# Kernel optimization log

Measured on AMD Instinct MI355X. Metric: run time of the kernel, lower is better.

## Reference

```python
import jax, jax.numpy as jnp
import numpy as np

B, T, D, H = 2, 2048, 1024, 16
DH = D // H  # 64


def setup_inputs() -> dict:
    key = jax.random.key(0)
    k1, k2, k3 = jax.random.split(key, 3)
    x = jax.random.normal(k1, (B, T, D), dtype=jnp.float32)
    # torch nn.Linear(d, 3d, bias=False): y = x @ W.T; we store W already transposed as [in, out]
    Wqkv = jax.random.normal(k2, (D, 3 * D), dtype=jnp.float32) * (1.0 / np.sqrt(D))
    Wproj = jax.random.normal(k3, (D, D), dtype=jnp.float32) * (1.0 / np.sqrt(D))
    return {"x": x, "Wqkv": Wqkv, "Wproj": Wproj}


def reference(x, Wqkv, Wproj):
    Bx, Tx, C = x.shape
    qkv = x @ Wqkv                                   # [B,T,3C]
    q, k, v = jnp.split(qkv, 3, axis=-1)
    def rs(t):
        return t.reshape(Bx, Tx, H, DH).transpose(0, 2, 1, 3)  # [B,H,T,DH]
    q, k, v = rs(q), rs(k), rs(v)
    scale = 1.0 / jnp.sqrt(jnp.asarray(DH, dtype=x.dtype))
    att = jnp.einsum('bhqd,bhkd->bhqk', q, k) * scale          # [B,H,T,T]
    causal = jnp.tril(jnp.ones((Tx, Tx), dtype=bool))
    att = jnp.where(causal[None, None, :, :], att, jnp.asarray(-jnp.inf, dtype=att.dtype))
    att = jax.nn.softmax(att, axis=-1)
    out = jnp.einsum('bhqk,bhkd->bhqd', att, v)                # [B,H,T,DH]
    out = out.transpose(0, 2, 1, 3).reshape(Bx, Tx, C)         # [B,T,C]
    return out @ Wproj
```

## Files before the change

kernel.cpp:

```cpp
#include <hip/hip_runtime.h>
#include <hip/hip_bf16.h>

#define BB 2
#define TT 2048
#define DD 1024
#define HH 16
#define MM (BB*TT)
#define N3 (3*DD)
#define QKW 2048

typedef __attribute__((ext_vector_type(8))) short short8;
typedef __attribute__((ext_vector_type(4))) float f32x4;
typedef __attribute__((ext_vector_type(16))) float f32x16;

#define ZERO16 (f32x16){0,0,0,0,0,0,0,0,0,0,0,0,0,0,0,0}

#define GLDS16(g, l) __builtin_amdgcn_global_load_lds( \
    (const __attribute__((address_space(1))) void*)(g), \
    (__attribute__((address_space(3))) void*)(l), 16, 0, 0)

__device__ __forceinline__ unsigned short f2bf(float f) {
    union { float f; unsigned u; } v; v.f = f;
    unsigned r = v.u + 0x7FFFu + ((v.u >> 16) & 1u);
    return (unsigned short)(r >> 16);
}

__device__ __forceinline__ unsigned cvt_pk_bf16(float lo, float hi) {
    unsigned r;
    asm("v_cvt_pk_bf16_f32 %0, %1, %2" : "=v"(r) : "v"(lo), "v"(hi));
    return r;
}

__device__ __forceinline__ float fast_exp2(float x) {
    float r;
    asm("v_exp_f32 %0, %1" : "=v"(r) : "v"(x));
    return r;
}
__device__ __forceinline__ float fast_rcp(float x) {
    float r;
    asm("v_rcp_f32 %0, %1" : "=v"(r) : "v"(x));
    return r;
}

__global__ void prep_kernel(const float* __restrict__ x,
                            const float* __restrict__ Wqkv,
                            const float* __restrict__ Wproj,
                            unsigned short* __restrict__ xb,
                            unsigned short* __restrict__ wqkvt,
                            unsigned short* __restrict__ wprojt) {
    __shared__ float tile[32][33];
    const int bid = blockIdx.x;
    const int tx = threadIdx.x, ty = threadIdx.y;
    if (bid < 4096) {
        const float* src;
        unsigned short* dst;
        int rows, cols, c0, r0;
        if (bid < 3072) {
            src = Wqkv; dst = wqkvt; rows = DD; cols = N3;
            c0 = (bid % 96) * 32; r0 = (bid / 96) * 32;
        } else {
            src = Wproj; dst = wprojt; rows = DD; cols = DD;
            int b2 = bid - 3072;
            c0 = (b2 & 31) * 32; r0 = (b2 >> 5) * 32;
        }
#pragma unroll
        for (int i = 0; i < 4; i++) {
            int r = ty + i * 8;
            tile[r][tx] = src[(size_t)(r0 + r) * cols + c0 + tx];
        }
        __syncthreads();
#pragma unroll
        for (int i = 0; i < 4; i++) {
            int r = ty + i * 8;
            dst[(size_t)(c0 + r) * rows + r0 + tx] = f2bf(tile[tx][r]);
        }
    } else {
        const int t = ty * 32 + tx;
        int i = (bid - 4096) * 256 + t;
        const int n8 = MM * DD / 8;
#pragma unroll
        for (int k = 0; k < 2; k++, i += 262144) {
            const float4* s = reinterpret_cast<const float4*>(x) + (size_t)i * 2;
            float4 a = s[0], b = s[1];
            unsigned short r[8] = {f2bf(a.x), f2bf(a.y), f2bf(a.z), f2bf(a.w),
                                   f2bf(b.x), f2bf(b.y), f2bf(b.z), f2bf(b.w)};
            *reinterpret_cast<uint4*>(xb + (size_t)i * 8) = *reinterpret_cast<uint4*>(r);
            (void)n8;
        }
    }
}

__global__ __launch_bounds__(512, 2)
void gemm256_qkv(const unsigned short* __restrict__ A,
                 const unsigned short* __restrict__ Bt,
                 unsigned short* __restrict__ qkv2,
                 unsigned short* __restrict__ Vout,
                 float scale) {
    __shared__ unsigned short Al[2][2][128][64];
    __shared__ unsigned short Bl[2][2][128][64];

    const int id = blockIdx.y * 12 + blockIdx.x;
    const int swzid = (id & 7) * 24 + (id >> 3);
    const int tm = (swzid / 12) * 256, tn = (swzid % 12) * 256;
    const int t = threadIdx.x, w = t >> 6, l = t & 63;
    const int wm = w >> 2, wn = w & 3, bh = wn >> 1;
    const int lo = l & 15, hi = l >> 4;
    const int srow = l >> 3;
    const int sg = (l & 7) ^ srow;

    f32x4 acc[8][4];
#pragma unroll
    for (int i = 0; i < 8; i++)
#pragma unroll
        for (int j = 0; j < 4; j++) acc[i][j] = (f32x4){0.f, 0.f, 0.f, 0.f};

    const unsigned short* Abase = A + (size_t)(tm + w * 16 + srow) * 1024 + sg * 8;
    const unsigned short* Bbase = Bt + (size_t)(tn + w * 16 + srow) * 1024 + sg * 8;

#define STG_A(KT, H) { \
    GLDS16(Abase + (size_t)(H) * 128 * 1024 + ((KT) & 15) * 64, &Al[(KT) & 1][H][w * 16][0]); \
    GLDS16(Abase + (size_t)(H) * 128 * 1024 + 8 * 1024 + ((KT) & 15) * 64, &Al[(KT) & 1][H][w * 16 + 8][0]); }
#define STG_B(KT, H) { \
    GLDS16(Bbase + (size_t)(H) * 128 * 1024 + ((KT) & 15) * 64, &Bl[(KT) & 1][H][w * 16][0]); \
    GLDS16(Bbase + (size_t)(H) * 128 * 1024 + 8 * 1024 + ((KT) & 15) * 64, &Bl[(KT) & 1][H][w * 16 + 8][0]); }

#define LOAD_A(AFR, KP, MH) { \
    const char* ab = (const char*)&Al[KP][wm][0][0]; \
    _Pragma("unroll") \
    for (int fi = 0; fi < 4; fi++) \
    _Pragma("unroll") \
    for (int ks = 0; ks < 2; ks++) \
        AFR[fi][ks] = *reinterpret_cast<const short8*>( \
            ab + ((MH) * 64 + fi * 16 + lo) * 128 + (((ks * 4 + hi) ^ (lo & 7)) << 4)); }
#define LOAD_B(BFR, KP, NH) { \
    const char* bb = (const char*)&Bl[KP][bh][0][0]; \
    _Pragma("unroll") \
    for (int fj = 0; fj < 2; fj++) \
    _Pragma("unroll") \
    for (int ks = 0; ks < 2; ks++) \
        BFR[fj][ks] = *reinterpret_cast<const short8*>( \
            bb + ((wn & 1) * 64 + (NH) * 32 + fj * 16 + lo) * 128 + (((ks * 4 + hi) ^ (lo & 7)) << 4)); }

#define MFMA16(MH, NH, AFR, BFR) { \
    _Pragma("unroll") \
    for (int ks = 0; ks < 2; ks++) \
    _Pragma("unroll") \
    for (int fi = 0; fi < 4; fi++) \
    _Pragma("unroll") \
    for (int fj = 0; fj < 2; fj++) \
        acc[(MH) * 4 + fi][(NH) * 2 + fj] = __builtin_amdgcn_mfma_f32_16x16x32_bf16( \
            AFR[fi][ks], BFR[fj][ks], acc[(MH) * 4 + fi][(NH) * 2 + fj], 0, 0, 0); }

#define BAR __builtin_amdgcn_s_barrier()
#define LGKM0 asm volatile("s_waitcnt lgkmcnt(0)")
#define P1 __builtin_amdgcn_s_setprio(1)
#define P0 __builtin_amdgcn_s_setprio(0)

    STG_A(0, 0); STG_A(0, 1); STG_B(0, 0); STG_B(0, 1);
    STG_B(1, 0); STG_B(1, 1);
    asm volatile("s_waitcnt vmcnt(4)");
    BAR;

    for (int i = 0; i < 8; i++) {
        const int kt = 2 * i;
        short8 AF[4][2], BA[2][2], BBf[2][2];
        LOAD_A(AF, 0, 0); LOAD_B(BA, 0, 0);
        STG_A(kt + 1, 0); STG_A(kt + 1, 1);
        BAR; LGKM0; P1; MFMA16(0, 0, AF, BA); P0; BAR;
        LOAD_B(BBf, 0, 1);
        BAR; LGKM0; P1; MFMA16(0, 1, AF, BBf); P0; BAR;
        LOAD_A(AF, 0, 1);
        STG_B(kt + 2, 0); STG_B(kt + 2, 1);
        BAR; LGKM0; P1; MFMA16(1, 1, AF, BBf); P0; BAR;
        STG_A(kt + 2, 0);
        BAR; LGKM0; P1; MFMA16(1, 0, AF, BA); P0;
        asm volatile("s_waitcnt vmcnt(6)");
        BAR;
        LOAD_A(AF, 1, 0); LOAD_B(BA, 1, 0);
        STG_A(kt + 2, 1);
        BAR; LGKM0; P1; MFMA16(0, 0, AF, BA); P0; BAR;
        LOAD_B(BBf, 1, 1);
        BAR; LGKM0; P1; MFMA16(0, 1, AF, BBf); P0; BAR;
        LOAD_A(AF, 1, 1);
        STG_B(kt + 3, 0); STG_B(kt + 3, 1);
        BAR; LGKM0; P1; MFMA16(1, 1, AF, BBf); P0; BAR;
        BAR; LGKM0; P1; MFMA16(1, 0, AF, BA); P0;
        asm volatile("s_waitcnt vmcnt(4)");
        BAR;
    }

#pragma unroll
    for (int i = 0; i < 8; i++)
#pragma unroll
        for (int j = 0; j < 4; j++) {
            const int col = tn + wn * 64 + j * 16 + lo;
            const int row0 = tm + wm * 128 + i * 16 + hi * 4;
            if (col < 2 * DD) {
                float s = (col < DD) ? scale : 1.0f;
#pragma unroll
                for (int r = 0; r < 4; r++)
                    qkv2[(size_t)(row0 + r) * QKW + col] = f2bf(acc[i][j][r] * s);
            } else {
                unsigned short pk[4];
#pragma unroll
                for (int r = 0; r < 4; r++) pk[r] = f2bf(acc[i][j][r]);
                *reinterpret_cast<uint2*>(&Vout[(size_t)(col - 2 * DD) * MM + row0]) =
                    *reinterpret_cast<uint2*>(pk);
            }
        }
#undef STG_A
#undef STG_B
#undef LOAD_A
#undef LOAD_B
#undef MFMA16
#undef BAR
#undef LGKM0
#undef P1
#undef P0
}

__global__ __launch_bounds__(256)
void gemm_kernel(const unsigned short* __restrict__ A,
                 const unsigned short* __restrict__ Bt,
                 float* __restrict__ Cout, int M, int N, int K) {
    __shared__ unsigned short As[128][64];
    __shared__ unsigned short Bs[128][64];
    const int nbx = gridDim.x;
    const int id = blockIdx.y * nbx + blockIdx.x;
    const int cpx = (nbx * gridDim.y) >> 3;
    const int swz = (id & 7) * cpx + (id >> 3);
    const int tm = (swz / nbx) * 128, tn = (swz % nbx) * 128;
    const int t = threadIdx.x;
    const int w = t >> 6, lane = t & 63, lo = lane & 15, hi = lane >> 4;
    const int wr = w >> 1, wc = w & 1;

    f32x4 acc[4][4];
#pragma unroll
    for (int i = 0; i < 4; i++)
#pragma unroll
        for (int j = 0; j < 4; j++) acc[i][j] = (f32x4){0.f, 0.f, 0.f, 0.f};

    const int srow = w * 32 + (lane >> 3);
    const int scol = (lane & 7) * 8;
    const unsigned short* ga = &A[(size_t)(tm + srow) * K + scol];
    const unsigned short* gb = &Bt[(size_t)(tn + srow) * K + scol];

    for (int k0 = 0; k0 < K; k0 += 64) {
        __syncthreads();
#pragma unroll
        for (int i = 0; i < 4; i++) {
            GLDS16(ga + (size_t)(i * 8) * K + k0, &As[w * 32 + i * 8][0]);
            GLDS16(gb + (size_t)(i * 8) * K + k0, &Bs[w * 32 + i * 8][0]);
        }
        __syncthreads();

        short8 af[4][2], bf[4][2];
#pragma unroll
        for (int i = 0; i < 4; i++)
#pragma unroll
            for (int ks = 0; ks < 2; ks++) {
                af[i][ks] = *reinterpret_cast<const short8*>(&As[wr * 64 + i * 16 + lo][ks * 32 + hi * 8]);
                bf[i][ks] = *reinterpret_cast<const short8*>(&Bs[wc * 64 + i * 16 + lo][ks * 32 + hi * 8]);
            }
#pragma unroll
        for (int ks = 0; ks < 2; ks++)
#pragma unroll
            for (int i = 0; i < 4; i++)
#pragma unroll
                for (int j = 0; j < 4; j++)
                    acc[i][j] = __builtin_amdgcn_mfma_f32_16x16x32_bf16(af[i][ks], bf[j][ks], acc[i][j], 0, 0, 0);
    }
#pragma unroll
    for (int i = 0; i < 4; i++)
#pragma unroll
        for (int j = 0; j < 4; j++) {
            const int col = tn + wc * 64 + j * 16 + lo;
            const int row0 = tm + wr * 64 + i * 16 + hi * 4;
#pragma unroll
            for (int r = 0; r < 4; r++)
                Cout[(size_t)(row0 + r) * N + col] = acc[i][j][r];
        }
}

__global__ __launch_bounds__(256)
void attn_kernel(const unsigned short* __restrict__ qkv2,
                 const unsigned short* __restrict__ vtg,
                 unsigned short* __restrict__ outp) {
    __shared__ unsigned short Ks[2][64][64];
    __shared__ unsigned short Vt[2][64][64];

    const int b = blockIdx.z, h = blockIdx.x, p = blockIdx.y;
    const int qcl = p, qch = 31 - p;
    const int L = p + 1, Hn = 32 - p;
    const int t = threadIdx.x;
    const int w = t >> 6, l = t & 63, ql = l & 31, hi8 = l >> 5;
    const int pr = w >> 1, rg = w & 1;
    const int q0h = qch * 64 + rg * 32;
    const int q0p = (pr ? qcl : qch) * 64 + rg * 32;
    const unsigned short* base2 = qkv2 + (size_t)b * TT * QKW;

    short8 bq[4];
#pragma unroll
    for (int ks = 0; ks < 4; ks++)
        bq[ks] = *reinterpret_cast<const short8*>(
            &base2[(size_t)(q0p + ql) * QKW + h * 64 + ks * 16 + hi8 * 8]);

    f32x16 o0 = ZERO16, o1 = ZERO16, lD = ZERO16;

    short8 ones1;
#pragma unroll
    for (int j = 0; j < 8; j++) ones1[j] = (short)0x3F80;

    const int krow = l >> 3;
    const int kc8 = (l & 7) ^ krow;
    const unsigned short* gk = &base2[(size_t)(w * 8 + krow) * QKW + DD + h * 64 + kc8 * 8];
    const unsigned short* gv = &vtg[(size_t)(h * 64 + w * 8 + krow) * MM + b * TT + kc8 * 8];

#define STAGE(KVB, BUF) { \
    GLDS16(gk + (size_t)(KVB) * QKW, &Ks[BUF][w * 8][0]); \
    GLDS16(gk + (size_t)((KVB) + 32) * QKW, &Ks[BUF][32 + w * 8][0]); \
    GLDS16(gv + (KVB), &Vt[BUF][w * 8][0]); \
    GLDS16(gv + (size_t)32 * MM + (KVB), &Vt[BUF][32 + w * 8][0]); }

#define WRITE_OUT(Q0) { \
    _Pragma("unroll") \
    for (int r = 0; r < 16; r++) { \
        int src = (r & 3) + 8 * (r >> 2) + 4 * hi8; \
        float inv = fast_rcp(lD[r]); \
        size_t off = (size_t)(b * TT + (Q0) + src) * DD + h * 64 + ql; \
        outp[off] = f2bf(o0[r] * inv); \
        outp[off + 32] = f2bf(o1[r] * inv); \
    } }

    STAGE(0, 0);
    __syncthreads();

    const int sw4 = (ql & 7) << 4;
    int it = 0;
    for (int kvt = 0; kvt < Hn; kvt++, it ^= 1) {
        const bool more = (kvt + 1) < Hn;
        if (more) STAGE((kvt + 1) * 64, it ^ 1);

        if (kvt == L && pr == 1) {
            WRITE_OUT(qcl * 64 + rg * 32);
            o0 = ZERO16; o1 = ZERO16; lD = ZERO16;
#pragma unroll
            for (int ks = 0; ks < 4; ks++)
                bq[ks] = *reinterpret_cast<const short8*>(
                    &base2[(size_t)(q0h + ql) * QKW + h * 64 + ks * 16 + hi8 * 8]);
        }

        const char* kbase = (const char*)&Ks[it][0][0];
        const char* vbase = (const char*)&Vt[it][0][0];
        const int kvb = kvt * 64;

        if (kvt < L) {
            short8 ak0[4], ak1[4];
#pragma unroll
            for (int ks = 0; ks < 4; ks++) {
                ak0[ks] = *reinterpret_cast<const short8*>(kbase + ql * 128 + (((ks * 2 + hi8) << 4) ^ sw4));
                ak1[ks] = *reinterpret_cast<const short8*>(kbase + (32 + ql) * 128 + (((ks * 2 + hi8) << 4) ^ sw4));
            }
            f32x16 sa0 = ZERO16, sa1 = ZERO16;
#pragma unroll
            for (int ks = 0; ks < 4; ks++) {
                sa0 = __builtin_amdgcn_mfma_f32_32x32x16_bf16(ak0[ks], bq[ks], sa0, 0, 0, 0);
                sa1 = __builtin_amdgcn_mfma_f32_32x32x16_bf16(ak1[ks], bq[ks], sa1, 0, 0, 0);
            }
            if (pr == 1 && kvt == L - 1) {
                const int qg = q0p + ql;
#pragma unroll
                for (int r = 0; r < 16; r++) {
                    int crow = (r & 3) + 8 * (r >> 2) + 4 * hi8;
                    if (kvb + crow > qg) sa0[r] = -1e30f;
                    if (kvb + 32 + crow > qg) sa1[r] = -1e30f;
                }
            }
#pragma unroll
            for (int r = 0; r < 16; r++) sa0[r] = fast_exp2(sa0[r]);
#pragma unroll
            for (int r = 0; r < 16; r++) sa1[r] = fast_exp2(sa1[r]);

            unsigned a01 = cvt_pk_bf16(sa0[0], sa0[1]),  a23 = cvt_pk_bf16(sa0[2], sa0[3]);
            unsigned a45 = cvt_pk_bf16(sa0[4], sa0[5]),  a67 = cvt_pk_bf16(sa0[6], sa0[7]);
            asm("v_permlane32_swap_b32 %0, %1" : "+v"(a01), "+v"(a45));
            asm("v_permlane32_swap_b32 %0, %1" : "+v"(a23), "+v"(a67));
            unsigned b01 = cvt_pk_bf16(sa0[8], sa0[9]),  b23 = cvt_pk_bf16(sa0[10], sa0[11]);
            unsigned b45 = cvt_pk_bf16(sa0[12], sa0[13]), b67 = cvt_pk_bf16(sa0[14], sa0[15]);
            asm("v_permlane32_swap_b32 %0, %1" : "+v"(b01), "+v"(b45));
            asm("v_permlane32_swap_b32 %0, %1" : "+v"(b23), "+v"(b67));
            unsigned c01 = cvt_pk_bf16(sa1[0], sa1[1]),  c23 = cvt_pk_bf16(sa1[2], sa1[3]);
            unsigned c45 = cvt_pk_bf16(sa1[4], sa1[5]),  c67 = cvt_pk_bf16(sa1[6], sa1[7]);
            asm("v_permlane32_swap_b32 %0, %1" : "+v"(c01), "+v"(c45));
            asm("v_permlane32_swap_b32 %0, %1" : "+v"(c23), "+v"(c67));
            unsigned d01 = cvt_pk_bf16(sa1[8], sa1[9]),  d23 = cvt_pk_bf16(sa1[10], sa1[11]);
            unsigned d45 = cvt_pk_bf16(sa1[12], sa1[13]), d67 = cvt_pk_bf16(sa1[14], sa1[15]);
            asm("v_permlane32_swap_b32 %0, %1" : "+v"(d01), "+v"(d45));
            asm("v_permlane32_swap_b32 %0, %1" : "+v"(d23), "+v"(d67));
            union { unsigned u[4]; short8 s; } f0s0, f1s0, f0s1, f1s1;
            f0s0.u[0] = a01; f0s0.u[1] = a23; f0s0.u[2] = a45; f0s0.u[3] = a67;
            f1s0.u[0] = b01; f1s0.u[1] = b23; f1s0.u[2] = b45; f1s0.u[3] = b67;
            f0s1.u[0] = c01; f0s1.u[1] = c23; f0s1.u[2] = c45; f0s1.u[3] = c67;
            f1s1.u[0] = d01; f1s1.u[1] = d23; f1s1.u[2] = d45; f1s1.u[3] = d67;

            lD = __builtin_amdgcn_mfma_f32_32x32x16_bf16(f0s0.s, ones1, lD, 0, 0, 0);
            lD = __builtin_amdgcn_mfma_f32_32x32x16_bf16(f1s0.s, ones1, lD, 0, 0, 0);
            lD = __builtin_amdgcn_mfma_f32_32x32x16_bf16(f0s1.s, ones1, lD, 0, 0, 0);
            lD = __builtin_amdgcn_mfma_f32_32x32x16_bf16(f1s1.s, ones1, lD, 0, 0, 0);

            short8 bv00 = *reinterpret_cast<const short8*>(vbase + ql * 128 + (((0 + hi8) << 4) ^ sw4));
            short8 bv01 = *reinterpret_cast<const short8*>(vbase + ql * 128 + (((2 + hi8) << 4) ^ sw4));
            short8 bv02 = *reinterpret_cast<const short8*>(vbase + ql * 128 + (((4 + hi8) << 4) ^ sw4));
            short8 bv03 = *reinterpret_cast<const short8*>(vbase + ql * 128 + (((6 + hi8) << 4) ^ sw4));
            short8 bv10 = *reinterpret_cast<const short8*>(vbase + (32 + ql) * 128 + (((0 + hi8) << 4) ^ sw4));
            short8 bv11 = *reinterpret_cast<const short8*>(vbase + (32 + ql) * 128 + (((2 + hi8) << 4) ^ sw4));
            short8 bv12 = *reinterpret_cast<const short8*>(vbase + (32 + ql) * 128 + (((4 + hi8) << 4) ^ sw4));
            short8 bv13 = *reinterpret_cast<const short8*>(vbase + (32 + ql) * 128 + (((6 + hi8) << 4) ^ sw4));
            o0 = __builtin_amdgcn_mfma_f32_32x32x16_bf16(f0s0.s, bv00, o0, 0, 0, 0);
            o1 = __builtin_amdgcn_mfma_f32_32x32x16_bf16(f0s0.s, bv10, o1, 0, 0, 0);
            o0 = __builtin_amdgcn_mfma_f32_32x32x16_bf16(f1s0.s, bv01, o0, 0, 0, 0);
            o1 = __builtin_amdgcn_mfma_f32_32x32x16_bf16(f1s0.s, bv11, o1, 0, 0, 0);
            o0 = __builtin_amdgcn_mfma_f32_32x32x16_bf16(f0s1.s, bv02, o0, 0, 0, 0);
            o1 = __builtin_amdgcn_mfma_f32_32x32x16_bf16(f0s1.s, bv12, o1, 0, 0, 0);
            o0 = __builtin_amdgcn_mfma_f32_32x32x16_bf16(f1s1.s, bv03, o0, 0, 0, 0);
            o1 = __builtin_amdgcn_mfma_f32_32x32x16_bf16(f1s1.s, bv13, o1, 0, 0, 0);
        } else {
            const int sub = pr;
            short8 ak[4];
#pragma unroll
            for (int ks = 0; ks < 4; ks++)
                ak[ks] = *reinterpret_cast<const short8*>(
                    kbase + (sub * 32 + ql) * 128 + (((ks * 2 + hi8) << 4) ^ sw4));
            f32x16 sa = ZERO16;
#pragma unroll
            for (int ks = 0; ks < 4; ks++)
                sa = __builtin_amdgcn_mfma_f32_32x32x16_bf16(ak[ks], bq[ks], sa, 0, 0, 0);

            if (kvt == Hn - 1) {
                const int qg = q0h + ql;
#pragma unroll
                for (int r = 0; r < 16; r++) {
                    int crow = (r & 3) + 8 * (r >> 2) + 4 * hi8;
                    if (kvb + sub * 32 + crow > qg) sa[r] = -1e30f;
                }
            }
#pragma unroll
            for (int r = 0; r < 16; r++) sa[r] = fast_exp2(sa[r]);

            unsigned a01 = cvt_pk_bf16(sa[0], sa[1]),  a23 = cvt_pk_bf16(sa[2], sa[3]);
            unsigned a45 = cvt_pk_bf16(sa[4], sa[5]),  a67 = cvt_pk_bf16(sa[6], sa[7]);
            asm("v_permlane32_swap_b32 %0, %1" : "+v"(a01), "+v"(a45));
            asm("v_permlane32_swap_b32 %0, %1" : "+v"(a23), "+v"(a67));
            unsigned b01 = cvt_pk_bf16(sa[8], sa[9]),  b23 = cvt_pk_bf16(sa[10], sa[11]);
            unsigned b45 = cvt_pk_bf16(sa[12], sa[13]), b67 = cvt_pk_bf16(sa[14], sa[15]);
            asm("v_permlane32_swap_b32 %0, %1" : "+v"(b01), "+v"(b45));
            asm("v_permlane32_swap_b32 %0, %1" : "+v"(b23), "+v"(b67));
            union { unsigned u[4]; short8 s; } f0, f1;
            f0.u[0] = a01; f0.u[1] = a23; f0.u[2] = a45; f0.u[3] = a67;
            f1.u[0] = b01; f1.u[1] = b23; f1.u[2] = b45; f1.u[3] = b67;

            lD = __builtin_amdgcn_mfma_f32_32x32x16_bf16(f0.s, ones1, lD, 0, 0, 0);
            lD = __builtin_amdgcn_mfma_f32_32x32x16_bf16(f1.s, ones1, lD, 0, 0, 0);

            short8 bv00 = *reinterpret_cast<const short8*>(vbase + ql * 128 + (((sub * 4 + 0 + hi8) << 4) ^ sw4));
            short8 bv01 = *reinterpret_cast<const short8*>(vbase + ql * 128 + (((sub * 4 + 2 + hi8) << 4) ^ sw4));
            short8 bv10 = *reinterpret_cast<const short8*>(vbase + (32 + ql) * 128 + (((sub * 4 + 0 + hi8) << 4) ^ sw4));
            short8 bv11 = *reinterpret_cast<const short8*>(vbase + (32 + ql) * 128 + (((sub * 4 + 2 + hi8) << 4) ^ sw4));
            o0 = __builtin_amdgcn_mfma_f32_32x32x16_bf16(f0.s, bv00, o0, 0, 0, 0);
            o1 = __builtin_amdgcn_mfma_f32_32x32x16_bf16(f0.s, bv10, o1, 0, 0, 0);
            o0 = __builtin_amdgcn_mfma_f32_32x32x16_bf16(f1.s, bv01, o0, 0, 0, 0);
            o1 = __builtin_amdgcn_mfma_f32_32x32x16_bf16(f1.s, bv11, o1, 0, 0, 0);
        }
        __syncthreads();
    }

    float* xf = (float*)&Ks[0][0][0];
    float* xl = (float*)&Vt[0][0][0];
    const int tid128 = (w & 1) * 64 + l;
    if (pr == 1) {
#pragma unroll
        for (int r = 0; r < 16; r++) {
            xf[r * 128 + tid128] = o0[r];
            xf[(16 + r) * 128 + tid128] = o1[r];
            xl[r * 128 + tid128] = lD[r];
        }
    }
    __syncthreads();
    if (pr == 0) {
#pragma unroll
        for (int r = 0; r < 16; r++) {
            o0[r] += xf[r * 128 + tid128];
            o1[r] += xf[(16 + r) * 128 + tid128];
            lD[r] += xl[r * 128 + tid128];
        }
        WRITE_OUT(q0h);
    }
#undef STAGE
#undef WRITE_OUT
}

extern "C" void kernel_launch(void* const* d_in, const int* in_sizes, int n_in,
                              void* d_out, int out_size, void* d_ws, size_t ws_size,
                              hipStream_t stream) {
    const float* x     = (const float*)d_in[0];
    const float* Wqkv  = (const float*)d_in[1];
    const float* Wproj = (const float*)d_in[2];
    float* out = (float*)d_out;

    unsigned short* xb     = (unsigned short*)d_ws;
    unsigned short* wqkvt  = xb + (size_t)MM * DD;
    unsigned short* wprojt = wqkvt + (size_t)N3 * DD;
    unsigned short* qkv2   = wprojt + (size_t)DD * DD;
    unsigned short* vtg    = qkv2 + (size_t)MM * QKW;
    unsigned short* attout = vtg + (size_t)DD * MM;
    size_t need = ((size_t)MM * DD + (size_t)N3 * DD + (size_t)DD * DD +
                   (size_t)MM * QKW + (size_t)DD * MM + (size_t)MM * DD) * 2;
    if (ws_size < need) return;

    const float sc = 0.125f * 1.44269504088896f;

    prep_kernel<<<5120, dim3(32, 8), 0, stream>>>(x, Wqkv, Wproj, xb, wqkvt, wprojt);

    gemm256_qkv<<<dim3(12, 16), 512, 0, stream>>>(xb, wqkvt, qkv2, vtg, sc);

    attn_kernel<<<dim3(HH, 16, BB), 256, 0, stream>>>(qkv2, vtg, attout);

    gemm_kernel<<<dim3(DD / 128, MM / 128), 256, 0, stream>>>(attout, wprojt, out, MM, DD, DD);
}
```

Baseline: 120.2 us.

## Triple-buffer attention K/V loads and retile projection GEMM to 128x64

```diff
diff --git a/kernel.cpp b/kernel.cpp
--- a/kernel.cpp
+++ b/kernel.cpp
@@ -77,7 +77,6 @@
     } else {
         const int t = ty * 32 + tx;
         int i = (bid - 4096) * 256 + t;
-        const int n8 = MM * DD / 8;
 #pragma unroll
         for (int k = 0; k < 2; k++, i += 262144) {
             const float4* s = reinterpret_cast<const float4*>(x) + (size_t)i * 2;
@@ -85,7 +84,6 @@
             unsigned short r[8] = {f2bf(a.x), f2bf(a.y), f2bf(a.z), f2bf(a.w),
                                    f2bf(b.x), f2bf(b.y), f2bf(b.z), f2bf(b.w)};
             *reinterpret_cast<uint4*>(xb + (size_t)i * 8) = *reinterpret_cast<uint4*>(r);
-            (void)n8;
         }
     }
 }
@@ -220,65 +218,69 @@
 }
 
 __global__ __launch_bounds__(256)
-void gemm_kernel(const unsigned short* __restrict__ A,
-                 const unsigned short* __restrict__ Bt,
-                 float* __restrict__ Cout, int M, int N, int K) {
+void gemm_proj(const unsigned short* __restrict__ A,
+               const unsigned short* __restrict__ Bt,
+               float* __restrict__ Cout) {
     __shared__ unsigned short As[128][64];
-    __shared__ unsigned short Bs[128][64];
-    const int nbx = gridDim.x;
+    __shared__ unsigned short Bs[64][64];
+    const int nbx = 16;
     const int id = blockIdx.y * nbx + blockIdx.x;
-    const int cpx = (nbx * gridDim.y) >> 3;
+    const int cpx = 512 >> 3;
     const int swz = (id & 7) * cpx + (id >> 3);
-    const int tm = (swz / nbx) * 128, tn = (swz % nbx) * 128;
+    const int tm = (swz / nbx) * 128, tn = (swz % nbx) * 64;
     const int t = threadIdx.x;
     const int w = t >> 6, lane = t & 63, lo = lane & 15, hi = lane >> 4;
     const int wr = w >> 1, wc = w & 1;
 
-    f32x4 acc[4][4];
+    f32x4 acc[4][2];
 #pragma unroll
     for (int i = 0; i < 4; i++)
 #pragma unroll
-        for (int j = 0; j < 4; j++) acc[i][j] = (f32x4){0.f, 0.f, 0.f, 0.f};
-
-    const int srow = w * 32 + (lane >> 3);
+        for (int j = 0; j < 2; j++) acc[i][j] = (f32x4){0.f, 0.f, 0.f, 0.f};
+
+    const int sr8 = lane >> 3;
     const int scol = (lane & 7) * 8;
-    const unsigned short* ga = &A[(size_t)(tm + srow) * K + scol];
-    const unsigned short* gb = &Bt[(size_t)(tn + srow) * K + scol];
-
-    for (int k0 = 0; k0 < K; k0 += 64) {
+    const unsigned short* ga = &A[(size_t)(tm + w * 32 + sr8) * 1024 + scol];
+    const unsigned short* gb = &Bt[(size_t)(tn + w * 16 + sr8) * 1024 + scol];
+
+    for (int k0 = 0; k0 < 1024; k0 += 64) {
         __syncthreads();
 #pragma unroll
-        for (int i = 0; i < 4; i++) {
-            GLDS16(ga + (size_t)(i * 8) * K + k0, &As[w * 32 + i * 8][0]);
-            GLDS16(gb + (size_t)(i * 8) * K + k0, &Bs[w * 32 + i * 8][0]);
-        }
+        for (int i = 0; i < 4; i++)
+            GLDS16(ga + (size_t)(i * 8) * 1024 + k0, &As[w * 32 + i * 8][0]);
+#pragma unroll
+        for (int i = 0; i < 2; i++)
+            GLDS16(gb + (size_t)(i * 8) * 1024 + k0, &Bs[w * 16 + i * 8][0]);
         __syncthreads();
 
-        short8 af[4][2], bf[4][2];
+        short8 af[4][2], bf[2][2];
 #pragma unroll
         for (int i = 0; i < 4; i++)
 #pragma unroll
-            for (int ks = 0; ks < 2; ks++) {
+            for (int ks = 0; ks < 2; ks++)
                 af[i][ks] = *reinterpret_cast<const short8*>(&As[wr * 64 + i * 16 + lo][ks * 32 + hi * 8]);
-                bf[i][ks] = *reinterpret_cast<const short8*>(&Bs[wc * 64 + i * 16 + lo][ks * 32 + hi * 8]);
-            }
+#pragma unroll
+        for (int j = 0; j < 2; j++)
+#pragma unroll
+            for (int ks = 0; ks < 2; ks++)
+                bf[j][ks] = *reinterpret_cast<const short8*>(&Bs[wc * 32 + j * 16 + lo][ks * 32 + hi * 8]);
 #pragma unroll
         for (int ks = 0; ks < 2; ks++)
 #pragma unroll
             for (int i = 0; i < 4; i++)
 #pragma unroll
-                for (int j = 0; j < 4; j++)
+                for (int j = 0; j < 2; j++)
                     acc[i][j] = __builtin_amdgcn_mfma_f32_16x16x32_bf16(af[i][ks], bf[j][ks], acc[i][j], 0, 0, 0);
     }
 #pragma unroll
     for (int i = 0; i < 4; i++)
 #pragma unroll
-        for (int j = 0; j < 4; j++) {
-            const int col = tn + wc * 64 + j * 16 + lo;
+        for (int j = 0; j < 2; j++) {
+            const int col = tn + wc * 32 + j * 16 + lo;
             const int row0 = tm + wr * 64 + i * 16 + hi * 4;
 #pragma unroll
             for (int r = 0; r < 4; r++)
-                Cout[(size_t)(row0 + r) * N + col] = acc[i][j][r];
+                Cout[(size_t)(row0 + r) * DD + col] = acc[i][j][r];
         }
 }
 
@@ -286,8 +288,8 @@
 void attn_kernel(const unsigned short* __restrict__ qkv2,
                  const unsigned short* __restrict__ vtg,
                  unsigned short* __restrict__ outp) {
-    __shared__ unsigned short Ks[2][64][64];
-    __shared__ unsigned short Vt[2][64][64];
+    __shared__ unsigned short Ks[3][64][64];
+    __shared__ unsigned short Vt[3][64][64];
 
     const int b = blockIdx.z, h = blockIdx.x, p = blockIdx.y;
     const int qcl = p, qch = 31 - p;
@@ -333,13 +335,15 @@
     } }
 
     STAGE(0, 0);
-    __syncthreads();
+    STAGE(64, 1);
+    asm volatile("s_waitcnt vmcnt(4)");
+    __builtin_amdgcn_s_barrier();
 
     const int sw4 = (ql & 7) << 4;
-    int it = 0;
-    for (int kvt = 0; kvt < Hn; kvt++, it ^= 1) {
-        const bool more = (kvt + 1) < Hn;
-        if (more) STAGE((kvt + 1) * 64, it ^ 1);
+    int cur = 0;
+    for (int kvt = 0; kvt < Hn; kvt++) {
+        const bool deep = (kvt + 2) < Hn;
+        if (deep) { STAGE((kvt + 2) * 64, cur == 0 ? 2 : cur - 1); }
 
         if (kvt == L && pr == 1) {
             WRITE_OUT(qcl * 64 + rg * 32);
@@ -350,8 +354,8 @@
                     &base2[(size_t)(q0h + ql) * QKW + h * 64 + ks * 16 + hi8 * 8]);
         }
 
-        const char* kbase = (const char*)&Ks[it][0][0];
-        const char* vbase = (const char*)&Vt[it][0][0];
+        const char* kbase = (const char*)&Ks[cur][0][0];
+        const char* vbase = (const char*)&Vt[cur][0][0];
         const int kvb = kvt * 64;
 
         if (kvt < L) {
@@ -471,7 +475,11 @@
             o0 = __builtin_amdgcn_mfma_f32_32x32x16_bf16(f1.s, bv01, o0, 0, 0, 0);
             o1 = __builtin_amdgcn_mfma_f32_32x32x16_bf16(f1.s, bv11, o1, 0, 0, 0);
         }
-        __syncthreads();
+
+        if (deep) asm volatile("s_waitcnt vmcnt(4)");
+        else if (kvt + 1 < Hn) asm volatile("s_waitcnt vmcnt(0)");
+        __builtin_amdgcn_s_barrier();
+        cur = (cur == 2) ? 0 : cur + 1;
     }
 
     float* xf = (float*)&Ks[0][0][0];
@@ -525,5 +533,5 @@
 
     attn_kernel<<<dim3(HH, 16, BB), 256, 0, stream>>>(qkv2, vtg, attout);
 
-    gemm_kernel<<<dim3(DD / 128, MM / 128), 256, 0, stream>>>(attout, wprojt, out, MM, DD, DD);
-}
+    gemm_proj<<<dim3(16, 32), 256, 0, stream>>>(attout, wprojt, out);
+}
```

After: 117.6 us. 2.1% less time.
